# Kernel optimization log

Hardware: AMD Instinct MI355X
Metric: run time of the kernel (lower is better)

The kernel has to match this reference:

```python
import jax, jax.numpy as jnp
import numpy as np

_pi = np.pi
CONST_FACTOR = jnp.asarray([
    1.0 / np.sqrt(4 * _pi),
    2 * _pi / 3 * np.sqrt(3 / (4 * _pi)),
    2 * _pi / 3 * np.sqrt(3 / (4 * _pi)),
    2 * _pi / 3 * np.sqrt(3 / (4 * _pi)),
    _pi / 4 * 3 * np.sqrt(5 / (12 * _pi)),
    _pi / 4 * 3 * np.sqrt(5 / (12 * _pi)),
    _pi / 4 * 3 * np.sqrt(5 / (12 * _pi)),
    _pi / 4 * (3.0 / 2) * np.sqrt(5 / (12 * _pi)),
    _pi / 4 * (1.0 / 2) * np.sqrt(5 / (4 * _pi))], dtype=np.float32)


def face_verts(verts, faces):
    # verts [B,V,3], faces [B,F,3] -> [B,F,3,3]
    B, V, _ = verts.shape
    flat = verts.reshape(-1, 3)
    idx = faces + (jnp.arange(B) * V)[:, None, None]
    return flat[idx.reshape(-1)].reshape(B, faces.shape[1], 3, 3)


def vertex_normals(verts, faces):
    # area-weighted vertex normals via scatter-add (matches the usual torch index_add_ impl)
    B, V, _ = verts.shape
    flat = verts.reshape(-1, 3)
    f = (faces + (jnp.arange(B) * V)[:, None, None]).reshape(-1, 3)
    vf = flat[f]  # [B*F, 3, 3]
    n = jnp.zeros_like(flat)
    n = n.at[f[:, 1]].add(jnp.cross(vf[:, 2] - vf[:, 1], vf[:, 0] - vf[:, 1]))
    n = n.at[f[:, 2]].add(jnp.cross(vf[:, 0] - vf[:, 2], vf[:, 1] - vf[:, 2]))
    n = n.at[f[:, 0]].add(jnp.cross(vf[:, 1] - vf[:, 0], vf[:, 2] - vf[:, 0]))
    n = n / jnp.maximum(jnp.linalg.norm(n, axis=1, keepdims=True), 1e-6)
    return n.reshape(B, V, 3)


def rasterize_gather(pix_to_face, bary_coords, attributes):
    # pix_to_face [N,H,W,K] packed indices (-1 = empty), bary [N,H,W,K,3], attributes [N,F,3,D]
    N, H, W, K = pix_to_face.shape
    D = attributes.shape[-1]
    mask = pix_to_face < 0
    vismask = (~mask).astype(attributes.dtype)
    idx = jnp.where(mask, 0, pix_to_face).reshape(-1)
    attr = attributes.reshape(-1, 3, D)
    pfv = attr[idx].reshape(N, H, W, K, 3, D)          # gather per-pixel face attrs
    pv = (bary_coords[..., None] * pfv).sum(-2)         # barycentric blend [N,H,W,K,D]
    pv = jnp.where(mask[..., None], 0.0, pv)
    pv = pv[:, :, :, 0].transpose(0, 3, 1, 2)           # [N,D,H,W]
    return jnp.concatenate([pv, vismask[:, :, :, 0][:, None]], axis=1)


def grid_sample_bilinear(img, grid):
    # img [N,C,H,W], grid [N,Ho,Wo,2] in [-1,1]; bilinear, zeros padding, align_corners=False
    N, C, H, W = img.shape
    gx = (grid[..., 0] + 1.0) * 0.5 * W - 0.5
    gy = (grid[..., 1] + 1.0) * 0.5 * H - 0.5
    x0 = jnp.floor(gx); y0 = jnp.floor(gy)
    x1 = x0 + 1; y1 = y0 + 1
    wx1 = gx - x0; wx0 = 1.0 - wx1
    wy1 = gy - y0; wy0 = 1.0 - wy1
    b = jnp.arange(N)[:, None, None]

    def gather(ix, iy):
        valid = (ix >= 0) & (ix <= W - 1) & (iy >= 0) & (iy <= H - 1)
        ixc = jnp.clip(ix, 0, W - 1).astype(jnp.int32)
        iyc = jnp.clip(iy, 0, H - 1).astype(jnp.int32)
        v = img[b, :, iyc, ixc]  # [N,Ho,Wo,C]
        return v * valid[..., None]

    out = (gather(x0, y0) * (wx0 * wy0)[..., None]
           + gather(x1, y0) * (wx1 * wy0)[..., None]
           + gather(x0, y1) * (wx0 * wy1)[..., None]
           + gather(x1, y1) * (wx1 * wy1)[..., None])
    return out.transpose(0, 3, 1, 2)  # [N,C,Ho,Wo]


def add_SHlight(normal_images, sh_coeff):
    # normal_images [N,3,H,W], sh_coeff [N,9,3]
    n = normal_images
    sh = jnp.stack([jnp.ones_like(n[:, 0]), n[:, 0], n[:, 1], n[:, 2],
                    n[:, 0] * n[:, 1], n[:, 0] * n[:, 2], n[:, 1] * n[:, 2],
                    n[:, 0] ** 2 - n[:, 1] ** 2, 3 * n[:, 2] ** 2 - 1.0], axis=1)
    sh = sh * CONST_FACTOR[None, :, None, None]
    return jnp.einsum('nkc,nkhw->nchw', sh_coeff, sh)


def setup_inputs() -> dict:
    key = jax.random.key(0)
    ks = jax.random.split(key, 8)
    B, V, F, H, W, UV = 4, 5000, 10000, 512, 512, 512
    vertices = jax.random.normal(ks[0], (B, V, 3), jnp.float32)
    transformed_vertices = jax.random.normal(ks[1], (B, V, 3), jnp.float32)
    albedos = jax.random.uniform(ks[2], (B, 3, UV, UV), jnp.float32)
    lights = jax.random.normal(ks[3], (B, 9, 3), jnp.float32)
    face_uvcoords = jax.random.uniform(ks[4], (1, F, 3, 3), jnp.float32, -1.0, 1.0)
    u = jax.random.uniform(ks[5], (B, H, W, 1, 3), jnp.float32, 1e-3, 1.0)
    bary_coords = u / u.sum(-1, keepdims=True)
    faces = jax.random.randint(ks[6], (1, F, 3), 0, V, jnp.int32)
    pix_to_face = jax.random.randint(ks[7], (B, H, W, 1), 0, B * F + 1, jnp.int32) - 1
    return {"vertices": vertices, "transformed_vertices": transformed_vertices,
            "albedos": albedos, "lights": lights, "face_uvcoords": face_uvcoords,
            "bary_coords": bary_coords, "faces": faces, "pix_to_face": pix_to_face}


def reference(vertices, transformed_vertices, albedos, lights, face_uvcoords, bary_coords, faces, pix_to_face):
    sg = jax.lax.stop_gradient
    B = vertices.shape[0]
    faces_b = jnp.broadcast_to(faces, (B,) + faces.shape[1:])
    tv = transformed_vertices.at[:, :, 2].add(10.0)
    fv = face_verts(vertices, faces_b)
    normals = vertex_normals(vertices, faces_b)
    fn = face_verts(normals, faces_b)
    tn = vertex_normals(tv, faces_b)
    tfn = face_verts(tn, faces_b)
    fuv = jnp.broadcast_to(face_uvcoords, (B,) + face_uvcoords.shape[1:])
    attributes = jnp.concatenate([fuv, sg(tfn), sg(fv), sg(fn)], axis=-1)  # [B,F,3,12]
    rendering = rasterize_gather(pix_to_face, bary_coords, attributes)     # [B,13,H,W]
    alpha_images = sg(rendering[:, -1:])
    grid = rendering[:, :3].transpose(0, 2, 3, 1)[..., :2]
    albedo_images = grid_sample_bilinear(albedos, grid)
    transformed_normal_map = sg(rendering[:, 3:6])
    pos_mask = (transformed_normal_map[:, 2:] < -0.05).astype(jnp.float32)
    normal_images = sg(rendering[:, 9:12])
    shading_images = add_SHlight(normal_images, lights)  # lights.shape[1]==9 -> SH path
    images = albedo_images * shading_images * alpha_images
    return images, albedo_images, alpha_images, pos_mask, shading_images, grid, normals
```

## Files before the change

kernel.cpp:

```cpp
#include <hip/hip_runtime.h>
#include <hip/hip_fp16.h>

namespace {

constexpr int B  = 4;
constexpr int V  = 5000;
constexpr int NF = 10000;
constexpr int H  = 512;
constexpr int W  = 512;
constexpr int HW = H * W;
constexpr int NPIX = B * HW;
constexpr int CAP = 32;
constexpr int BNF = B * NF;
constexpr int BV  = B * V;

constexpr int OFF_IMAGES  = 0;
constexpr int OFF_ALBEDO  = 3 * NPIX;
constexpr int OFF_ALPHA   = OFF_ALBEDO + 3 * NPIX;
constexpr int OFF_POSMASK = OFF_ALPHA + NPIX;
constexpr int OFF_SHADING = OFF_POSMASK + NPIX;
constexpr int OFF_GRID    = OFF_SHADING + 3 * NPIX;
constexpr int OFF_NORMALS = OFF_GRID + 2 * NPIX;

constexpr float C0 = 0.28209479177387814f;
constexpr float C1 = 1.0233267079464885f;
constexpr float C4 = 0.8580855308097834f;
constexpr float C7 = 0.42904276540489156f;
constexpr float C8 = 0.24770795610037571f;

__device__ inline float pack_h2(float a, float b) {
    __half2 h = __floats2half2_rn(a, b);
    float r;
    *reinterpret_cast<__half2*>(&r) = h;
    return r;
}
__device__ inline float2 unpack_h2(float fbits) {
    __half2 h = *reinterpret_cast<__half2*>(&fbits);
    return __half22float2(h);
}
__device__ inline unsigned pack_h2u(float a, float b) {
    __half2 h = __floats2half2_rn(a, b);
    unsigned r;
    *reinterpret_cast<__half2*>(&r) = h;
    return r;
}
__device__ inline float2 unpack_h2u(unsigned ubits) {
    __half2 h = *reinterpret_cast<__half2*>(&ubits);
    return __half22float2(h);
}

__global__ __launch_bounds__(256) void bigfill_k(
    const int*   __restrict__ faces,
    const float* __restrict__ fuv,
    const float* __restrict__ verts,
    const float* __restrict__ tverts,
    const float* __restrict__ albedo,
    int*         __restrict__ cnt,
    int*         __restrict__ keys,
    float4*      __restrict__ fng,
    float4*      __restrict__ fnt,
    float*       __restrict__ ftab,
    uint2*       __restrict__ apack) {
    int gid = blockIdx.x * 256 + threadIdx.x;
    if (gid < NPIX) {
        int b = gid >> 18, hw = gid & (HW - 1);
        const float* ab = albedo + (size_t)b * 3 * HW;
        uint2 t;
        t.x = pack_h2u(ab[hw], ab[HW + hw]);
        t.y = pack_h2u(ab[2*HW + hw], 0.0f);
        apack[gid] = t;
        return;
    }
    int i = gid - NPIX;
    if (i >= BNF) return;
    int b = i / NF, f = i - b * NF;
    int j0 = faces[f*3+0], j1 = faces[f*3+1], j2 = faces[f*3+2];

    {
        const float* vb = verts + (size_t)b * V * 3;
        float x0 = vb[j0*3], y0 = vb[j0*3+1], z0 = vb[j0*3+2];
        float x1 = vb[j1*3], y1 = vb[j1*3+1], z1 = vb[j1*3+2];
        float x2 = vb[j2*3], y2 = vb[j2*3+1], z2 = vb[j2*3+2];
        {
            float ax=x2-x1, ay=y2-y1, az=z2-z1, bx=x0-x1, by=y0-y1, bz=z0-z1;
            fng[0*BNF + i] = make_float4(ay*bz - az*by, az*bx - ax*bz, ax*by - ay*bx, 0.f);
        }
        {
            float ax=x0-x2, ay=y0-y2, az=z0-z2, bx=x1-x2, by=y1-y2, bz=z1-z2;
            fng[1*BNF + i] = make_float4(ay*bz - az*by, az*bx - ax*bz, ax*by - ay*bx, 0.f);
        }
        {
            float ax=x1-x0, ay=y1-y0, az=z1-z0, bx=x2-x0, by=y2-y0, bz=z2-z0;
            fng[2*BNF + i] = make_float4(ay*bz - az*by, az*bx - ax*bz, ax*by - ay*bx, 0.f);
        }
    }
    {
        const float* tb = tverts + (size_t)b * V * 3;
        float x0 = tb[j0*3], y0 = tb[j0*3+1], z0 = tb[j0*3+2] + 10.0f;
        float x1 = tb[j1*3], y1 = tb[j1*3+1], z1 = tb[j1*3+2] + 10.0f;
        float x2 = tb[j2*3], y2 = tb[j2*3+1], z2 = tb[j2*3+2] + 10.0f;
        {
            float ax=x2-x1, ay=y2-y1, az=z2-z1, bx=x0-x1, by=y0-y1, bz=z0-z1;
            fnt[0*BNF + i] = make_float4(ay*bz - az*by, az*bx - ax*bz, ax*by - ay*bx, 0.f);
        }
        {
            float ax=x0-x2, ay=y0-y2, az=z0-z2, bx=x1-x2, by=y1-y2, bz=z1-z2;
            fnt[1*BNF + i] = make_float4(ay*bz - az*by, az*bx - ax*bz, ax*by - ay*bx, 0.f);
        }
        {
            float ax=x1-x0, ay=y1-y0, az=z1-z0, bx=x2-x0, by=y2-y0, bz=z2-z0;
            fnt[2*BNF + i] = make_float4(ay*bz - az*by, az*bx - ax*bz, ax*by - ay*bx, 0.f);
        }
    }
    const float* uv = fuv + (size_t)f * 9;
    float* row = ftab + (size_t)i * 16;
    *(float4*)(row + 0) = make_float4(uv[0], uv[1], uv[3], uv[4]);
    *(float2*)(row + 4) = make_float2(uv[6], uv[7]);
    if (i < NF) {
        int p;
        p = atomicAdd(&cnt[j1], 1); if (p < CAP) keys[j1*CAP + p] = 0*NF + f;
        p = atomicAdd(&cnt[j2], 1); if (p < CAP) keys[j2*CAP + p] = 1*NF + f;
        p = atomicAdd(&cnt[j0], 1); if (p < CAP) keys[j0*CAP + p] = 2*NF + f;
    }
}

__global__ __launch_bounds__(256) void vsum_k(
    const int*    __restrict__ cnt,
    const int*    __restrict__ keys,
    const float4* __restrict__ fng,
    const float4* __restrict__ fnt,
    float*        __restrict__ normV,
    float4*       __restrict__ vng,
    float*        __restrict__ tnzA) {
    int id = blockIdx.x * 256 + threadIdx.x;
    if (id >= 2 * BV) return;
    int half = (id >= BV) ? 1 : 0;
    int i = id - half * BV;
    int b = i / V, v = i - b * V;

    int n = min(cnt[v], CAP);
    int ks[CAP];
    const int4* kp = (const int4*)(keys + (size_t)v * CAP);
#pragma unroll
    for (int j = 0; j < CAP/4; ++j) {
        int4 t = kp[j];
        ks[4*j+0] = t.x; ks[4*j+1] = t.y; ks[4*j+2] = t.z; ks[4*j+3] = t.w;
    }
#pragma unroll
    for (int j = 0; j < CAP; ++j) ks[j] = (j < n) ? ks[j] : 0x7fffffff;

    const float4* src = half ? fnt : fng;
    float sx = 0.f, sy = 0.f, sz = 0.f;
    int last = -1;
    for (int e = 0; e < n; ++e) {
        int cur = 0x7fffffff;
#pragma unroll
        for (int j = 0; j < CAP; ++j) {
            int k = ks[j];
            bool g = (k > last) && (k < cur);
            cur = g ? k : cur;
        }
        last = cur;
        int phase = (cur >= 2*NF) ? 2 : (cur >= NF ? 1 : 0);
        int f = cur - phase * NF;
        float4 t = src[phase * BNF + b * NF + f];
        sx += t.x; sy += t.y; sz += t.z;
    }
    float inv = 1.0f / fmaxf(sqrtf(sx*sx + sy*sy + sz*sz), 1e-6f);
    if (half == 0) {
        sx *= inv; sy *= inv; sz *= inv;
        normV[i*3+0] = sx; normV[i*3+1] = sy; normV[i*3+2] = sz;
        vng[i] = make_float4(sx, sy, sz, 0.f);
    } else {
        tnzA[i] = sz * inv;
    }
}

__global__ __launch_bounds__(256) void fpack_k(
    const int*    __restrict__ faces,
    const float4* __restrict__ vng,
    const float*  __restrict__ tnzA,
    float*        __restrict__ ftab) {
    int i = blockIdx.x * 256 + threadIdx.x;
    if (i >= BNF) return;
    int b = i / NF, f = i - b * NF;
    int j0 = faces[f*3+0], j1 = faces[f*3+1], j2 = faces[f*3+2];
    int g0 = b*V + j0, g1 = b*V + j1, g2 = b*V + j2;
    float4 n0 = vng[g0], n1 = vng[g1], n2 = vng[g2];
    float t0 = tnzA[g0], t1 = tnzA[g1], t2 = tnzA[g2];
    float* row = ftab + (size_t)i * 16;
    *(float4*)(row + 6)  = make_float4(t0, t1, t2, pack_h2(n0.x, n0.y));
    *(float4*)(row + 10) = make_float4(pack_h2(n0.z, n1.x), pack_h2(n1.y, n1.z),
                                       pack_h2(n2.x, n2.y), pack_h2(n2.z, 0.f));
}

struct PixR { float u, v, s0, s1, s2, a0, a1, a2, vis, tz; };

__device__ inline PixR shade_px(int f, float b0, float b1, float b2, int b,
                                const float* __restrict__ ftab,
                                const uint2* __restrict__ apack,
                                const float* __restrict__ L) {
    PixR r;
    r.vis = (f >= 0) ? 1.0f : 0.0f;
    int fs = (f >= 0) ? f : 0;
    float w0 = b0 * r.vis, w1 = b1 * r.vis, w2 = b2 * r.vis;
    const float4* fr = (const float4*)(ftab + (size_t)fs * 16);
    float4 qa = fr[0];
    float4 qb = fr[1];
    float4 qc = fr[2];
    float2 qd = *(const float2*)(ftab + (size_t)fs * 16 + 12);
    r.u  = w0*qa.x + w1*qa.z + w2*qb.x;
    r.v  = w0*qa.y + w1*qa.w + w2*qb.y;
    r.tz = w0*qb.z + w1*qb.w + w2*qc.x;
    float2 p0 = unpack_h2(qc.y);
    float2 p1 = unpack_h2(qc.z);
    float2 p2 = unpack_h2(qc.w);
    float2 p3 = unpack_h2(qd.x);
    float2 p4 = unpack_h2(qd.y);
    float nx = w0*p0.x + w1*p1.y + w2*p3.x;
    float ny = w0*p0.y + w1*p2.x + w2*p3.y;
    float nz = w0*p1.x + w1*p2.y + w2*p4.x;

    float shb[9] = {C0, C1*nx, C1*ny, C1*nz, C4*nx*ny, C4*nx*nz, C4*ny*nz,
                    C7*(nx*nx - ny*ny), C8*(3.0f*nz*nz - 1.0f)};
    float s0 = 0.0f, s1 = 0.0f, s2 = 0.0f;
#pragma unroll
    for (int k = 0; k < 9; ++k) {
        float sk = shb[k];
        s0 += L[k*3+0]*sk; s1 += L[k*3+1]*sk; s2 += L[k*3+2]*sk;
    }
    r.s0 = s0; r.s1 = s1; r.s2 = s2;

    float gx = (r.u + 1.0f) * 0.5f * (float)W - 0.5f;
    float gy = (r.v + 1.0f) * 0.5f * (float)H - 0.5f;
    float x0 = floorf(gx), y0 = floorf(gy);
    float wx1 = gx - x0, wx0 = 1.0f - wx1;
    float wy1 = gy - y0, wy0 = 1.0f - wy1;
    float a0 = 0.0f, a1 = 0.0f, a2 = 0.0f;
    float fx[4] = {x0, x0 + 1.0f, x0,        x0 + 1.0f};
    float fy[4] = {y0, y0,        y0 + 1.0f, y0 + 1.0f};
    float wt[4] = {wx0*wy0, wx1*wy0, wx0*wy1, wx1*wy1};
#pragma unroll
    for (int c = 0; c < 4; ++c) {
        bool valid = (fx[c] >= 0.0f) && (fx[c] <= (float)(W-1)) &&
                     (fy[c] >= 0.0f) && (fy[c] <= (float)(H-1));
        if (valid) {
            int ix = (int)fx[c];
            int iy = (int)fy[c];
            uint2 t = apack[(b << 18) + iy * W + ix];
            float2 rg = unpack_h2u(t.x);
            float2 bz = unpack_h2u(t.y);
            float wgt = wt[c];
            a0 += wgt * rg.x; a1 += wgt * rg.y; a2 += wgt * bz.x;
        }
    }
    r.a0 = a0; r.a1 = a1; r.a2 = a2;
    return r;
}

__global__ __launch_bounds__(256) void pixel_k(
    const int*    __restrict__ ptf,
    const float*  __restrict__ bary,
    const uint2*  __restrict__ apack,
    const float*  __restrict__ lights,
    const float*  __restrict__ ftab,
    float*        __restrict__ out) {
    int bid = blockIdx.x;
    int dataBid = (bid & 7) * (NPIX / 512 / 8) + (bid >> 3);
    int pix = dataBid * 512 + threadIdx.x * 2;
    int b  = pix >> 18;
    int hw = pix & (HW - 1);

    int2 ff = *(const int2*)(ptf + pix);
    const float2* b2 = (const float2*)(bary + (size_t)pix * 3);
    float2 ba = b2[0], bb = b2[1], bc = b2[2];
    const float* L = lights + (size_t)__builtin_amdgcn_readfirstlane(b) * 27;

    PixR A = shade_px(ff.x, ba.x, ba.y, bb.x, b, ftab, apack, L);
    PixR Bx = shade_px(ff.y, bb.y, bc.x, bc.y, b, ftab, apack, L);

    int obase = b * 3 * HW + hw;
    *(float2*)(out + OFF_IMAGES + obase       ) = make_float2(A.a0*A.s0*A.vis, Bx.a0*Bx.s0*Bx.vis);
    *(float2*)(out + OFF_IMAGES + obase +  HW ) = make_float2(A.a1*A.s1*A.vis, Bx.a1*Bx.s1*Bx.vis);
    *(float2*)(out + OFF_IMAGES + obase + 2*HW) = make_float2(A.a2*A.s2*A.vis, Bx.a2*Bx.s2*Bx.vis);
    *(float2*)(out + OFF_ALBEDO + obase       ) = make_float2(A.a0, Bx.a0);
    *(float2*)(out + OFF_ALBEDO + obase +  HW ) = make_float2(A.a1, Bx.a1);
    *(float2*)(out + OFF_ALBEDO + obase + 2*HW) = make_float2(A.a2, Bx.a2);
    *(float2*)(out + OFF_ALPHA   + pix) = make_float2(A.vis, Bx.vis);
    *(float2*)(out + OFF_POSMASK + pix) = make_float2(A.tz < -0.05f ? 1.0f : 0.0f,
                                                      Bx.tz < -0.05f ? 1.0f : 0.0f);
    *(float2*)(out + OFF_SHADING + obase       ) = make_float2(A.s0, Bx.s0);
    *(float2*)(out + OFF_SHADING + obase +  HW ) = make_float2(A.s1, Bx.s1);
    *(float2*)(out + OFF_SHADING + obase + 2*HW) = make_float2(A.s2, Bx.s2);
    *(float4*)(out + OFF_GRID + (size_t)pix*2) = make_float4(A.u, A.v, Bx.u, Bx.v);
}

}

extern "C" void kernel_launch(void* const* d_in, const int* in_sizes, int n_in,
                              void* d_out, int out_size, void* d_ws, size_t ws_size,
                              hipStream_t stream) {
    const float* verts  = (const float*)d_in[0];
    const float* tverts = (const float*)d_in[1];
    const float* albedo = (const float*)d_in[2];
    const float* lights = (const float*)d_in[3];
    const float* fuv    = (const float*)d_in[4];
    const float* bary   = (const float*)d_in[5];
    const int*   faces  = (const int*)d_in[6];
    const int*   ptf    = (const int*)d_in[7];
    float* out = (float*)d_out;

    char* ws = (char*)d_ws;
    int*    cnt   = (int*)ws;
    int*    keys  = cnt + V;
    float4* vng   = (float4*)(((uintptr_t)(keys + (size_t)V*CAP) + 255) & ~(uintptr_t)255);
    float*  tnzA  = (float*)(vng + BV);
    char*   pend  = (char*)(tnzA + BV);
    size_t base      = (size_t)(pend - ws);
    size_t fng_off   = (base + 255) & ~(size_t)255;
    size_t fnt_off   = (fng_off + (size_t)3*BNF*sizeof(float4) + 255) & ~(size_t)255;
    size_t ftab_off  = (fnt_off + (size_t)3*BNF*sizeof(float4) + 255) & ~(size_t)255;
    size_t apack_off = (ftab_off + (size_t)BNF*16*sizeof(float) + 255) & ~(size_t)255;
    float4* fng   = (float4*)(ws + fng_off);
    float4* fnt   = (float4*)(ws + fnt_off);
    float*  ftab  = (float*)(ws + ftab_off);
    uint2*  apack = (uint2*)(ws + apack_off);
    float* normV = out + OFF_NORMALS;

    hipMemsetAsync(cnt, 0, (size_t)V * sizeof(int), stream);
    bigfill_k<<<(NPIX + BNF + 255)/256, 256, 0, stream>>>(faces, fuv, verts, tverts,
                                                          albedo, cnt, keys, fng, fnt,
                                                          ftab, apack);
    vsum_k<<<(2*BV + 255)/256, 256, 0, stream>>>(cnt, keys, fng, fnt, normV, vng, tnzA);
    fpack_k<<<(BNF + 255)/256, 256, 0, stream>>>(faces, vng, tnzA, ftab);
    pixel_k<<<NPIX/512, 256, 0, stream>>>(ptf, bary, apack, lights, ftab, out);
}
```

Measured before the change: 78.45 us.

## Process four pixels per thread and move adjacency fill into separate kernel

The pixel kernel now handles four consecutive pixels per thread, using int4/float4 loads of face ids and barycentrics and float4 stores for every output plane, which halves the block count and widens memory transactions. The per-vertex adjacency atomics move out of the big fill kernel into a small dedicated kernel, and the counter zeroing is folded into the fill kernel instead of a separate memset. The aim is to cut launch/memset overhead and raise store and load efficiency, in exchange for more registers per thread and an extra kernel launch.

```diff
diff --git a/kernel.cpp b/kernel.cpp
--- a/kernel.cpp
+++ b/kernel.cpp
@@ -56,12 +56,12 @@
     const float* __restrict__ tverts,
     const float* __restrict__ albedo,
     int*         __restrict__ cnt,
-    int*         __restrict__ keys,
     float4*      __restrict__ fng,
     float4*      __restrict__ fnt,
     float*       __restrict__ ftab,
     uint2*       __restrict__ apack) {
     int gid = blockIdx.x * 256 + threadIdx.x;
+    if (gid < V) cnt[gid] = 0;
     if (gid < NPIX) {
         int b = gid >> 18, hw = gid & (HW - 1);
         const float* ab = albedo + (size_t)b * 3 * HW;
@@ -116,12 +116,17 @@
     float* row = ftab + (size_t)i * 16;
     *(float4*)(row + 0) = make_float4(uv[0], uv[1], uv[3], uv[4]);
     *(float2*)(row + 4) = make_float2(uv[6], uv[7]);
-    if (i < NF) {
-        int p;
-        p = atomicAdd(&cnt[j1], 1); if (p < CAP) keys[j1*CAP + p] = 0*NF + f;
-        p = atomicAdd(&cnt[j2], 1); if (p < CAP) keys[j2*CAP + p] = 1*NF + f;
-        p = atomicAdd(&cnt[j0], 1); if (p < CAP) keys[j0*CAP + p] = 2*NF + f;
-    }
+}
+
+__global__ void fill_k(const int* __restrict__ faces, int* __restrict__ cnt,
+                       int* __restrict__ keys) {
+    int f = blockIdx.x * blockDim.x + threadIdx.x;
+    if (f >= NF) return;
+    int j0 = faces[f*3+0], j1 = faces[f*3+1], j2 = faces[f*3+2];
+    int p;
+    p = atomicAdd(&cnt[j1], 1); if (p < CAP) keys[j1*CAP + p] = 0*NF + f;
+    p = atomicAdd(&cnt[j2], 1); if (p < CAP) keys[j2*CAP + p] = 1*NF + f;
+    p = atomicAdd(&cnt[j0], 1); if (p < CAP) keys[j0*CAP + p] = 2*NF + f;
 }
 
 __global__ __launch_bounds__(256) void vsum_k(
@@ -266,33 +271,40 @@
     const float*  __restrict__ ftab,
     float*        __restrict__ out) {
     int bid = blockIdx.x;
-    int dataBid = (bid & 7) * (NPIX / 512 / 8) + (bid >> 3);
-    int pix = dataBid * 512 + threadIdx.x * 2;
+    int dataBid = (bid & 7) * (NPIX / 1024 / 8) + (bid >> 3);
+    int pix = dataBid * 1024 + threadIdx.x * 4;
     int b  = pix >> 18;
     int hw = pix & (HW - 1);
 
-    int2 ff = *(const int2*)(ptf + pix);
-    const float2* b2 = (const float2*)(bary + (size_t)pix * 3);
-    float2 ba = b2[0], bb = b2[1], bc = b2[2];
+    int4 ff = *(const int4*)(ptf + pix);
+    const float4* b4 = (const float4*)(bary + (size_t)pix * 3);
+    float4 c0 = b4[0], c1 = b4[1], c2 = b4[2];
     const float* L = lights + (size_t)__builtin_amdgcn_readfirstlane(b) * 27;
 
-    PixR A = shade_px(ff.x, ba.x, ba.y, bb.x, b, ftab, apack, L);
-    PixR Bx = shade_px(ff.y, bb.y, bc.x, bc.y, b, ftab, apack, L);
+    PixR P0 = shade_px(ff.x, c0.x, c0.y, c0.z, b, ftab, apack, L);
+    PixR P1 = shade_px(ff.y, c0.w, c1.x, c1.y, b, ftab, apack, L);
+    PixR P2 = shade_px(ff.z, c1.z, c1.w, c2.x, b, ftab, apack, L);
+    PixR P3 = shade_px(ff.w, c2.y, c2.z, c2.w, b, ftab, apack, L);
 
     int obase = b * 3 * HW + hw;
-    *(float2*)(out + OFF_IMAGES + obase       ) = make_float2(A.a0*A.s0*A.vis, Bx.a0*Bx.s0*Bx.vis);
-    *(float2*)(out + OFF_IMAGES + obase +  HW ) = make_float2(A.a1*A.s1*A.vis, Bx.a1*Bx.s1*Bx.vis);
-    *(float2*)(out + OFF_IMAGES + obase + 2*HW) = make_float2(A.a2*A.s2*A.vis, Bx.a2*Bx.s2*Bx.vis);
-    *(float2*)(out + OFF_ALBEDO + obase       ) = make_float2(A.a0, Bx.a0);
-    *(float2*)(out + OFF_ALBEDO + obase +  HW ) = make_float2(A.a1, Bx.a1);
-    *(float2*)(out + OFF_ALBEDO + obase + 2*HW) = make_float2(A.a2, Bx.a2);
-    *(float2*)(out + OFF_ALPHA   + pix) = make_float2(A.vis, Bx.vis);
-    *(float2*)(out + OFF_POSMASK + pix) = make_float2(A.tz < -0.05f ? 1.0f : 0.0f,
-                                                      Bx.tz < -0.05f ? 1.0f : 0.0f);
-    *(float2*)(out + OFF_SHADING + obase       ) = make_float2(A.s0, Bx.s0);
-    *(float2*)(out + OFF_SHADING + obase +  HW ) = make_float2(A.s1, Bx.s1);
-    *(float2*)(out + OFF_SHADING + obase + 2*HW) = make_float2(A.s2, Bx.s2);
-    *(float4*)(out + OFF_GRID + (size_t)pix*2) = make_float4(A.u, A.v, Bx.u, Bx.v);
+    *(float4*)(out + OFF_IMAGES + obase       ) = make_float4(
+        P0.a0*P0.s0*P0.vis, P1.a0*P1.s0*P1.vis, P2.a0*P2.s0*P2.vis, P3.a0*P3.s0*P3.vis);
+    *(float4*)(out + OFF_IMAGES + obase +  HW ) = make_float4(
+        P0.a1*P0.s1*P0.vis, P1.a1*P1.s1*P1.vis, P2.a1*P2.s1*P2.vis, P3.a1*P3.s1*P3.vis);
+    *(float4*)(out + OFF_IMAGES + obase + 2*HW) = make_float4(
+        P0.a2*P0.s2*P0.vis, P1.a2*P1.s2*P1.vis, P2.a2*P2.s2*P2.vis, P3.a2*P3.s2*P3.vis);
+    *(float4*)(out + OFF_ALBEDO + obase       ) = make_float4(P0.a0, P1.a0, P2.a0, P3.a0);
+    *(float4*)(out + OFF_ALBEDO + obase +  HW ) = make_float4(P0.a1, P1.a1, P2.a1, P3.a1);
+    *(float4*)(out + OFF_ALBEDO + obase + 2*HW) = make_float4(P0.a2, P1.a2, P2.a2, P3.a2);
+    *(float4*)(out + OFF_ALPHA   + pix) = make_float4(P0.vis, P1.vis, P2.vis, P3.vis);
+    *(float4*)(out + OFF_POSMASK + pix) = make_float4(
+        P0.tz < -0.05f ? 1.0f : 0.0f, P1.tz < -0.05f ? 1.0f : 0.0f,
+        P2.tz < -0.05f ? 1.0f : 0.0f, P3.tz < -0.05f ? 1.0f : 0.0f);
+    *(float4*)(out + OFF_SHADING + obase       ) = make_float4(P0.s0, P1.s0, P2.s0, P3.s0);
+    *(float4*)(out + OFF_SHADING + obase +  HW ) = make_float4(P0.s1, P1.s1, P2.s1, P3.s1);
+    *(float4*)(out + OFF_SHADING + obase + 2*HW) = make_float4(P0.s2, P1.s2, P2.s2, P3.s2);
+    *(float4*)(out + OFF_GRID + (size_t)pix*2    ) = make_float4(P0.u, P0.v, P1.u, P1.v);
+    *(float4*)(out + OFF_GRID + (size_t)pix*2 + 4) = make_float4(P2.u, P2.v, P3.u, P3.v);
 }
 
 }
@@ -327,11 +339,11 @@
     uint2*  apack = (uint2*)(ws + apack_off);
     float* normV = out + OFF_NORMALS;
 
-    hipMemsetAsync(cnt, 0, (size_t)V * sizeof(int), stream);
     bigfill_k<<<(NPIX + BNF + 255)/256, 256, 0, stream>>>(faces, fuv, verts, tverts,
-                                                          albedo, cnt, keys, fng, fnt,
+                                                          albedo, cnt, fng, fnt,
                                                           ftab, apack);
+    fill_k<<<(NF + 255)/256, 256, 0, stream>>>(faces, cnt, keys);
     vsum_k<<<(2*BV + 255)/256, 256, 0, stream>>>(cnt, keys, fng, fnt, normV, vng, tnzA);
     fpack_k<<<(BNF + 255)/256, 256, 0, stream>>>(faces, vng, tnzA, ftab);
-    pixel_k<<<NPIX/512, 256, 0, stream>>>(ptf, bary, apack, lights, ftab, out);
-}
+    pixel_k<<<NPIX/1024, 256, 0, stream>>>(ptf, bary, apack, lights, ftab, out);
+}
```

Measured after the change: 78.13 us. Within noise of the previous version (-0.4%).
